# Kernel optimization log

Hardware: AMD Instinct MI355X
Metric: run time of the kernel (lower is better)

The kernel has to match this reference:

```python
import jax, jax.numpy as jnp
import numpy as np

B, T, FEATS, HEAD = 2, 2048, 2048, 16
DIM_HEAD = FEATS // HEAD
EPS = float(jnp.finfo(jnp.float32).eps)  # torch nn.RMSNorm default eps=None -> dtype eps


def _rms_norm(u, g):
    # u: [..., d]; torch RMSNorm: u / sqrt(mean(u^2) + eps) * g
    return u * jax.lax.rsqrt(jnp.mean(u * u, axis=-1, keepdims=True) + EPS) * g


def setup_inputs() -> dict:
    key = jax.random.key(0)
    kx, kw = jax.random.split(key)
    x = jax.random.normal(kx, (B, T, FEATS), dtype=jnp.float32)
    W = jax.random.normal(kw, (FEATS, FEATS), dtype=jnp.float32) / np.sqrt(FEATS)
    g1 = jnp.ones((DIM_HEAD,), dtype=jnp.float32)
    g2 = jnp.ones((DIM_HEAD,), dtype=jnp.float32)
    g3 = jnp.ones((DIM_HEAD,), dtype=jnp.float32)
    return {"x": x, "W": W, "g1": g1, "g2": g2, "g3": g3}


def reference(x, W, g1, g2, g3):
    Bb, Tt, C = x.shape
    sqrt_d = jnp.asarray(DIM_HEAD ** 0.5, dtype=x.dtype)
    # tied QKV projection: torch Linear -> x @ W.T ; then split heads -> [B,H,T,D]
    w = (x @ W.T).reshape(Bb, Tt, HEAD, DIM_HEAD).transpose(0, 2, 1, 3)
    q = _rms_norm(w, g1)
    k = _rms_norm(w, g2)
    v = _rms_norm(w, g3)
    att = jnp.einsum("bhid,bhjd->bhij", q, k) / sqrt_d  # [B,H,T,T]
    # symmetric row + column softmax
    score = jax.nn.softmax(att, axis=-1) + jax.nn.softmax(att, axis=-2)
    y = jnp.einsum("bhij,bhjd->bihd", score, v).reshape(Bb, Tt, C)
    # F.linear(y, W.t()) == y @ W  (tied-weight reprojection)
    return y @ W
```

## Files before the change

kernel.cpp:

```cpp
#include <hip/hip_runtime.h>
#include <stdint.h>

#define T_SEQ 2048
#define B_SZ 2
#define N_HEAD 16
#define D_HEAD 128
#define C_DIM 2048
#define M_ROWS (B_SZ*T_SEQ)
#define N_BH (B_SZ*N_HEAD)

typedef _Float16 f16;
typedef f16 f16x8 __attribute__((ext_vector_type(8)));
typedef f16 f16x4 __attribute__((ext_vector_type(4)));
typedef float f32x4 __attribute__((ext_vector_type(4)));

#define MFMA_F16(a,b,c) __builtin_amdgcn_mfma_f32_16x16x32_f16(a,b,c,0,0,0)

#define BAR_LGKM() do { asm volatile("s_waitcnt lgkmcnt(0)" ::: "memory"); \
                        __builtin_amdgcn_s_barrier(); } while (0)
#define BAR_ALL()  do { asm volatile("s_waitcnt vmcnt(0) lgkmcnt(0)" ::: "memory"); \
                        __builtin_amdgcn_s_barrier(); } while (0)

__device__ __forceinline__ float fexp2(float x) {
#if __has_builtin(__builtin_amdgcn_exp2f)
  return __builtin_amdgcn_exp2f(x);
#else
  float r; asm("v_exp_f32 %0, %1" : "=v"(r) : "v"(x)); return r;
#endif
}

__device__ __forceinline__ void gl_lds16(const void* g, void* l) {
  __builtin_amdgcn_global_load_lds(
      (const __attribute__((address_space(1))) unsigned int*)g,
      (__attribute__((address_space(3))) unsigned int*)l, 16, 0, 0);
}

#define MB_SCALE 0.12752924444069595f
#define RMS_EPS  1.1920928955078125e-07f

__global__ void k_prep(const float* __restrict__ W, const float* __restrict__ x,
                       f16* __restrict__ Wb, f16* __restrict__ Wtb,
                       f16* __restrict__ xb) {
  __shared__ float tile[64][65];
  const int lin = blockIdx.x;
  const int t = threadIdx.x;
  if (lin < 1024) {
    const int bx = (lin & 31) * 64;
    const int by = (lin >> 5) * 64;
    const int tc = t & 63, tr4 = t >> 6;
    for (int rr = tr4; rr < 64; rr += 4) {
      float v = W[(size_t)(by + rr) * C_DIM + bx + tc];
      tile[rr][tc] = v;
      Wb[(size_t)(by + rr) * C_DIM + bx + tc] = (f16)v;
    }
    __syncthreads();
    for (int rr = tr4; rr < 64; rr += 4) {
      Wtb[(size_t)(bx + rr) * C_DIM + by + tc] = (f16)tile[tc][rr];
    }
  } else {
    int i = (lin - 1024) * 256 + t;
    const int stride = 2048 * 256;
    const int n4 = (M_ROWS * C_DIM) / 4;
    for (; i < n4; i += stride) {
      f32x4 v = ((const f32x4*)x)[i];
      f16x4 o; o[0]=(f16)v[0]; o[1]=(f16)v[1]; o[2]=(f16)v[2]; o[3]=(f16)v[3];
      ((f16x4*)xb)[i] = o;
    }
  }
}

template<typename OT>
__global__ __launch_bounds__(256, 2)
void k_gemm_bt(const f16* __restrict__ A, const f16* __restrict__ Bm,
               OT* __restrict__ C, int Nd, int Kd) {
  __shared__ __align__(16) f16 As[2][128 * 64];
  __shared__ __align__(16) f16 Bs[2][128 * 64];
  const int tid = threadIdx.x;
  const int lane = tid & 63, wid = tid >> 6;
  const int lr = lane & 15, lkg = lane >> 4;
  const int wr = wid >> 1, wc = wid & 1;
  const int tm = blockIdx.y * 128, tn = blockIdx.x * 128;

  f32x4 acc[4][4];
#pragma unroll
  for (int i = 0; i < 4; ++i)
#pragma unroll
    for (int j = 0; j < 4; ++j) acc[i][j] = (f32x4){0.f, 0.f, 0.f, 0.f};

  const int nkt = Kd >> 6;

  auto stage = [&](int buf, int kt) {
    const int k0 = kt << 6;
    for (int s = 0; s < 4; ++s) {
      const int r0 = (wid * 4 + s) * 8;
      const int r = r0 + (lane >> 3);
      const int lg = ((lane & 7) ^ (r & 7)) << 3;
      gl_lds16(A + (size_t)(tm + r) * Kd + k0 + lg, &As[buf][r0 * 64]);
      gl_lds16(Bm + (size_t)(tn + r) * Kd + k0 + lg, &Bs[buf][r0 * 64]);
    }
  };

  stage(0, 0);
  int cur = 0;
  for (int kt = 0; kt < nkt; ++kt) {
    __syncthreads();
    if (kt + 1 < nkt) stage(cur ^ 1, kt + 1);
#pragma unroll
    for (int kk = 0; kk < 2; ++kk) {
      f16x8 a[4], b[4];
#pragma unroll
      for (int i = 0; i < 4; ++i) {
        const int ra = wr * 64 + i * 16 + lr;
        const int ga = ((kk * 4 + lkg) ^ (ra & 7)) << 3;
        a[i] = *(const f16x8*)&As[cur][ra * 64 + ga];
        const int rb = wc * 64 + i * 16 + lr;
        const int gb = ((kk * 4 + lkg) ^ (rb & 7)) << 3;
        b[i] = *(const f16x8*)&Bs[cur][rb * 64 + gb];
      }
#pragma unroll
      for (int i = 0; i < 4; ++i)
#pragma unroll
        for (int j = 0; j < 4; ++j) acc[i][j] = MFMA_F16(a[i], b[j], acc[i][j]);
    }
    cur ^= 1;
  }
#pragma unroll
  for (int i = 0; i < 4; ++i) {
    const int row0 = tm + wr * 64 + i * 16 + lkg * 4;
#pragma unroll
    for (int j = 0; j < 4; ++j) {
      const int col = tn + wc * 64 + j * 16 + lr;
#pragma unroll
      for (int r = 0; r < 4; ++r)
        C[(size_t)(row0 + r) * Nd + col] = (OT)acc[i][j][r];
    }
  }
}

__global__ __launch_bounds__(256, 2)
void k_gemm_qkv(const f16* __restrict__ A, const f16* __restrict__ Bm,
                const float* __restrict__ g1, const float* __restrict__ g2,
                f16* __restrict__ nb, f16* __restrict__ mb,
                f16* __restrict__ nT) {
  __shared__ __align__(16) char smem[70656];
  f16 (*As)[128 * 64] = (f16(*)[128 * 64])smem;
  f16 (*Bs)[128 * 64] = (f16(*)[128 * 64])(smem + 32768);
  f16* Cs = (f16*)smem;
  float* sc = (float*)(smem + 69632);

  const int tid = threadIdx.x;
  const int lane = tid & 63, wid = tid >> 6;
  const int lr = lane & 15, lkg = lane >> 4;
  const int wr = wid >> 1, wc = wid & 1;
  const int tm = blockIdx.y * 128;
  const int hh = blockIdx.x;
  const int tn = hh * 128;

  f32x4 acc[4][4];
#pragma unroll
  for (int i = 0; i < 4; ++i)
#pragma unroll
    for (int j = 0; j < 4; ++j) acc[i][j] = (f32x4){0.f, 0.f, 0.f, 0.f};

  auto stage = [&](int buf, int kt) {
    const int k0 = kt << 6;
    for (int s = 0; s < 4; ++s) {
      const int r0 = (wid * 4 + s) * 8;
      const int r = r0 + (lane >> 3);
      const int lg = ((lane & 7) ^ (r & 7)) << 3;
      gl_lds16(A + (size_t)(tm + r) * C_DIM + k0 + lg, &As[buf][r0 * 64]);
      gl_lds16(Bm + (size_t)(tn + r) * C_DIM + k0 + lg, &Bs[buf][r0 * 64]);
    }
  };

  stage(0, 0);
  int cur = 0;
  for (int kt = 0; kt < 32; ++kt) {
    __syncthreads();
    if (kt + 1 < 32) stage(cur ^ 1, kt + 1);
#pragma unroll
    for (int kk = 0; kk < 2; ++kk) {
      f16x8 a[4], b[4];
#pragma unroll
      for (int i = 0; i < 4; ++i) {
        const int ra = wr * 64 + i * 16 + lr;
        const int ga = ((kk * 4 + lkg) ^ (ra & 7)) << 3;
        a[i] = *(const f16x8*)&As[cur][ra * 64 + ga];
        const int rb = wc * 64 + i * 16 + lr;
        const int gb = ((kk * 4 + lkg) ^ (rb & 7)) << 3;
        b[i] = *(const f16x8*)&Bs[cur][rb * 64 + gb];
      }
#pragma unroll
      for (int i = 0; i < 4; ++i)
#pragma unroll
        for (int j = 0; j < 4; ++j) acc[i][j] = MFMA_F16(a[i], b[j], acc[i][j]);
    }
    cur ^= 1;
  }
  __syncthreads();

#pragma unroll
  for (int i = 0; i < 4; ++i)
#pragma unroll
    for (int j = 0; j < 4; ++j)
#pragma unroll
      for (int r = 0; r < 4; ++r)
        Cs[(wr * 64 + i * 16 + lkg * 4 + r) * 136 + wc * 64 + j * 16 + lr] =
            (f16)acc[i][j][r];
  __syncthreads();

  const int row = tid >> 1, dh = tid & 1;
  f16x8 v[8];
  float ss = 0.f;
#pragma unroll
  for (int c = 0; c < 8; ++c) {
    v[c] = *(const f16x8*)&Cs[row * 136 + dh * 64 + c * 8];
#pragma unroll
    for (int e = 0; e < 8; ++e) { float f = (float)v[c][e]; ss += f * f; }
  }
  ss += __shfl_xor(ss, 1);
  const float scale = rsqrtf(ss * (1.f / 128.f) + RMS_EPS);
  if (dh == 0) sc[row] = scale;

  const int grow = tm + row;
  const int b = grow >> 11, ts = grow & (T_SEQ - 1);
  const size_t nbase =
      ((size_t)((b * N_HEAD + hh) * T_SEQ + ts)) * 128 + dh * 64;
#pragma unroll
  for (int c = 0; c < 8; ++c) {
    const int d0 = dh * 64 + c * 8;
    f16x8 n8, m8;
#pragma unroll
    for (int e = 0; e < 8; ++e) {
      const float nf = (float)v[c][e] * scale;
      n8[e] = (f16)nf;
      m8[e] = (f16)(nf * g1[d0 + e] * g2[d0 + e] * MB_SCALE);
    }
    *(f16x8*)&nb[nbase + c * 8] = n8;
    *(f16x8*)&mb[nbase + c * 8] = m8;
  }
  __syncthreads();

  const int dcol = tid >> 1, th = tid & 1;
  const size_t tbase =
      ((size_t)((b * N_HEAD + hh) * 128 + dcol)) * T_SEQ + (tm & (T_SEQ - 1)) +
      th * 64;
#pragma unroll
  for (int rr = 0; rr < 8; ++rr) {
    f16x8 o;
#pragma unroll
    for (int e = 0; e < 8; ++e) {
      const int trow = th * 64 + rr * 8 + e;
      o[e] = (f16)((float)Cs[trow * 136 + dcol] * sc[trow]);
    }
    *(f16x8*)&nT[tbase + rr * 8] = o;
  }
}

__global__ __launch_bounds__(256, 2)
void k_stats_strip(const f16* __restrict__ mIn, const f16* __restrict__ nIn,
                   float* __restrict__ Ssum) {
  __shared__ __align__(16) f16 Ns[2][128 * 128];
  const int tid = threadIdx.x, lane = tid & 63, wid = tid >> 6;
  const int lr = lane & 15, lkg = lane >> 4;
  const int wr = wid >> 1, wc = wid & 1;
  const int p = blockIdx.x >> 1, h = blockIdx.x & 1;
  const int it1 = p, it2 = 15 - p;
  const int n1 = 16 - p;
  const int bh = blockIdx.y;
  const f16* mp = mIn + (size_t)bh * T_SEQ * 128;
  const f16* np = nIn + (size_t)bh * T_SEQ * 128;
  float* Sp = Ssum + (size_t)bh * T_SEQ;

  f16x8 msrW[2][4];
  auto loadMsr = [&](int itv) {
#pragma unroll
    for (int i = 0; i < 2; ++i)
#pragma unroll
      for (int kk = 0; kk < 4; ++kk)
        msrW[i][kk] = *(const f16x8*)&mp[(size_t)(itv * 128 + h * 64 + wr * 32 +
                                                  i * 16 + lr) * 128 +
                                         (kk * 4 + lkg) * 8];
  };
  auto stageN = [&](int buf, int jt) {
#pragma unroll
    for (int s = 0; s < 8; ++s) {
      const int r0 = (wid * 8 + s) * 4;
      const int r = r0 + (lane >> 4);
      const int lg = ((lane & 15) ^ (r & 7)) << 3;
      gl_lds16(np + (size_t)(jt * 128 + r) * 128 + lg, &Ns[buf][r0 * 128]);
    }
  };

  float rsum[8];
#pragma unroll
  for (int q = 0; q < 8; ++q) rsum[q] = 0.f;
  auto flushRows = [&](int itv) {
#pragma unroll
    for (int q = 0; q < 8; ++q) {
      float v = rsum[q];
      v += __shfl_xor(v, 1); v += __shfl_xor(v, 2);
      v += __shfl_xor(v, 4); v += __shfl_xor(v, 8);
      if (lr == 0) {
        const int row = itv * 128 + h * 64 + wr * 32 + (q >> 2) * 16 +
                        lkg * 4 + (q & 3);
        atomicAdd(&Sp[row], v);
      }
      rsum[q] = 0.f;
    }
  };

  loadMsr(it1);
  stageN(0, it1);
  BAR_ALL();
  int cur = 0;
  float csumP[4];
  int jtP = -1;

  for (int s = 0; s < 17; ++s) {
    const int itv = (s < n1) ? it1 : it2;
    const int jt = (s < n1) ? (it1 + s) : (it2 + (s - n1));
    if (s + 1 < 17) {
      const int jn = (s + 1 < n1) ? (it1 + s + 1) : (it2 + (s + 1 - n1));
      stageN(cur ^ 1, jn);
    }
    if (jtP >= 0) {
#pragma unroll
      for (int j = 0; j < 4; ++j)
        if (lkg == 0)
          atomicAdd(&Sp[jtP * 128 + wc * 64 + j * 16 + lr], csumP[j]);
      jtP = -1;
    }
    if (s == n1) { loadMsr(it2); flushRows(it1); }

    f32x4 acc[2][4];
#pragma unroll
    for (int i = 0; i < 2; ++i)
#pragma unroll
      for (int j = 0; j < 4; ++j) acc[i][j] = (f32x4){0.f, 0.f, 0.f, 0.f};
#pragma unroll
    for (int kk = 0; kk < 4; ++kk) {
      f16x8 b[4];
#pragma unroll
      for (int j = 0; j < 4; ++j) {
        const int rb = wc * 64 + j * 16 + lr;
        const int gb = ((kk * 4 + lkg) ^ (rb & 7)) << 3;
        b[j] = *(const f16x8*)&Ns[cur][rb * 128 + gb];
      }
#pragma unroll
      for (int i = 0; i < 2; ++i)
#pragma unroll
        for (int j = 0; j < 4; ++j)
          acc[i][j] = MFMA_F16(msrW[i][kk], b[j], acc[i][j]);
    }
    float cs[4];
#pragma unroll
    for (int j = 0; j < 4; ++j) cs[j] = 0.f;
#pragma unroll
    for (int i = 0; i < 2; ++i)
#pragma unroll
      for (int j = 0; j < 4; ++j)
#pragma unroll
        for (int r = 0; r < 4; ++r) {
          const float e = fexp2(acc[i][j][r]);
          rsum[i * 4 + r] += e;
          cs[j] += e;
        }
    if (jt != itv) {
#pragma unroll
      for (int j = 0; j < 4; ++j) {
        float v = cs[j];
        v += __shfl_xor(v, 16); v += __shfl_xor(v, 32);
        csumP[j] = v;
      }
      jtP = jt;
    }
    BAR_ALL();
    cur ^= 1;
  }
  if (jtP >= 0) {
#pragma unroll
    for (int j = 0; j < 4; ++j)
      if (lkg == 0)
        atomicAdd(&Sp[jtP * 128 + wc * 64 + j * 16 + lr], csumP[j]);
  }
  flushRows(it2);
}

__global__ void k_inv(const float* __restrict__ S, float* __restrict__ alpha) {
  const int i = blockIdx.x * blockDim.x + threadIdx.x;
  f32x4 s = ((const f32x4*)S)[i];
  f32x4 a;
#pragma unroll
  for (int e = 0; e < 4; ++e) a[e] = 1.f / s[e];
  ((f32x4*)alpha)[i] = a;
}

__global__ __launch_bounds__(256, 2)
void k_apply(const f16* __restrict__ mIn, const f16* __restrict__ nIn,
             const f16* __restrict__ nTIn, const float* __restrict__ alpha,
             const float* __restrict__ g3, f16* __restrict__ yb) {
  __shared__ __align__(16) f16 Ns[2][64 * 128];
  __shared__ __align__(16) f16 Nts[2][128 * 64];
  __shared__ __align__(16) f16 Ps[128 * 64];
  const int tid = threadIdx.x, lane = tid & 63, wid = tid >> 6;
  const int lr = lane & 15, lkg = lane >> 4;
  const int wj = wid >> 1;
  const int wi = wid & 1;
  const int lin = blockIdx.x + (blockIdx.y << 4);
  const int swz = ((lin & 7) << 6) + (lin >> 3);
  const int it = swz & 15, bh = swz >> 4;
  const int b = bh >> 4, hh = bh & 15;
  const f16* mp = mIn + (size_t)bh * T_SEQ * 128;
  const f16* np = nIn + (size_t)bh * T_SEQ * 128;
  const f16* ntp = nTIn + (size_t)bh * 128 * T_SEQ;
  const float* al = alpha + (size_t)bh * T_SEQ;

  f16x8 msr[4][4];
#pragma unroll
  for (int ii = 0; ii < 4; ++ii)
#pragma unroll
    for (int kk = 0; kk < 4; ++kk)
      msr[ii][kk] = *(const f16x8*)&mp[(size_t)(it * 128 + wi * 64 + ii * 16 + lr) * 128 +
                                       (kk * 4 + lkg) * 8];

  auto stageN = [&](int buf, int jt) {
#pragma unroll
    for (int s = 0; s < 4; ++s) {
      const int r0 = (wid * 4 + s) * 4;
      const int r = r0 + (lane >> 4);
      const int lg = ((lane & 15) ^ (r & 7)) << 3;
      gl_lds16(np + (size_t)(jt * 64 + r) * 128 + lg, &Ns[buf][r0 * 128]);
    }
  };
  auto stageNT = [&](int buf, int jt) {
#pragma unroll
    for (int s = 0; s < 4; ++s) {
      const int r0 = (wid * 4 + s) * 8;
      const int r = r0 + (lane >> 3);
      const int lg = ((lane & 7) ^ (r & 7)) << 3;
      gl_lds16(ntp + (size_t)r * T_SEQ + jt * 64 + lg, &Nts[buf][r0 * 64]);
    }
  };

  float ai[4];
#pragma unroll
  for (int ii = 0; ii < 4; ++ii) ai[ii] = al[it * 128 + wi * 64 + ii * 16 + lr];

  f32x4 yacc[4][4];
#pragma unroll
  for (int i = 0; i < 4; ++i)
#pragma unroll
    for (int j = 0; j < 4; ++j) yacc[i][j] = (f32x4){0.f, 0.f, 0.f, 0.f};

  stageN(0, 0);
  stageNT(0, 0);
  BAR_ALL();
  int cur = 0;
  for (int jt = 0; jt < 32; ++jt) {
    float aj[8];
#pragma unroll
    for (int jj = 0; jj < 2; ++jj)
#pragma unroll
      for (int r = 0; r < 4; ++r)
        aj[jj * 4 + r] = al[jt * 64 + wj * 32 + jj * 16 + lkg * 4 + r];
    if (jt < 31) { stageN(cur ^ 1, jt + 1); stageNT(cur ^ 1, jt + 1); }

    f32x4 acc[2][4];
#pragma unroll
    for (int i = 0; i < 2; ++i)
#pragma unroll
      for (int j = 0; j < 4; ++j) acc[i][j] = (f32x4){0.f, 0.f, 0.f, 0.f};
#pragma unroll
    for (int kk = 0; kk < 4; ++kk) {
      f16x8 a[2];
#pragma unroll
      for (int jj = 0; jj < 2; ++jj) {
        const int jrow = wj * 32 + jj * 16 + lr;
        a[jj] = *(const f16x8*)&Ns[cur][jrow * 128 + (((kk * 4 + lkg) ^ (jrow & 7)) << 3)];
      }
#pragma unroll
      for (int jj = 0; jj < 2; ++jj)
#pragma unroll
        for (int ii = 0; ii < 4; ++ii)
          acc[jj][ii] = MFMA_F16(a[jj], msr[ii][kk], acc[jj][ii]);
    }

#pragma unroll
    for (int jj = 0; jj < 2; ++jj)
#pragma unroll
      for (int ii = 0; ii < 4; ++ii) {
        f16x4 o;
#pragma unroll
        for (int r = 0; r < 4; ++r) {
          const float p = fexp2(acc[jj][ii][r]) * (ai[ii] + aj[jj * 4 + r]);
          o[r] = (f16)p;
        }
        const int il = wi * 64 + ii * 16 + lr;
        const int jl = wj * 32 + jj * 16 + lkg * 4;
        *(f16x4*)&Ps[il * 64 + (((jl >> 3) ^ (il & 7)) << 3) + (jl & 7)] = o;
      }
    BAR_LGKM();

#pragma unroll
    for (int kk = 0; kk < 2; ++kk) {
      f16x8 a[4], bfr[4];
#pragma unroll
      for (int dd = 0; dd < 4; ++dd) {
        const int drow = wj * 64 + dd * 16 + lr;
        a[dd] = *(const f16x8*)&Nts[cur][drow * 64 + (((kk * 4 + lkg) ^ (drow & 7)) << 3)];
      }
#pragma unroll
      for (int ii = 0; ii < 4; ++ii) {
        const int irow = wi * 64 + ii * 16 + lr;
        bfr[ii] = *(const f16x8*)&Ps[irow * 64 + (((kk * 4 + lkg) ^ (irow & 7)) << 3)];
      }
#pragma unroll
      for (int dd = 0; dd < 4; ++dd)
#pragma unroll
        for (int ii = 0; ii < 4; ++ii)
          yacc[dd][ii] = MFMA_F16(a[dd], bfr[ii], yacc[dd][ii]);
    }
    BAR_ALL();
    cur ^= 1;
  }

#pragma unroll
  for (int dd = 0; dd < 4; ++dd) {
    const int d0 = wj * 64 + dd * 16 + lkg * 4;
    float g3v[4];
#pragma unroll
    for (int r = 0; r < 4; ++r) g3v[r] = g3[d0 + r];
#pragma unroll
    for (int ii = 0; ii < 4; ++ii) {
      const int icol = wi * 64 + ii * 16 + lr;
      const size_t base =
          ((size_t)(b * T_SEQ + it * 128 + icol)) * C_DIM + hh * 128 + d0;
      f16x4 o;
#pragma unroll
      for (int r = 0; r < 4; ++r) o[r] = (f16)(yacc[dd][ii][r] * g3v[r]);
      *(f16x4*)&yb[base] = o;
    }
  }
}

extern "C" void kernel_launch(void* const* d_in, const int* in_sizes, int n_in,
                              void* d_out, int out_size, void* d_ws,
                              size_t ws_size, hipStream_t stream) {
  const float* x = (const float*)d_in[0];
  const float* W = (const float*)d_in[1];
  const float* g1 = (const float*)d_in[2];
  const float* g2 = (const float*)d_in[3];
  const float* g3 = (const float*)d_in[4];
  float* out = (float*)d_out;
  char* ws = (char*)d_ws;

  f16* xb   = (f16*)(ws);
  f16* Wb   = (f16*)(ws + 16777216);
  f16* Wtb  = (f16*)(ws + 25165824);
  f16* nb   = (f16*)(ws + 50331648);
  f16* mb   = (f16*)(ws + 67108864);
  f16* nT   = (f16*)(ws + 83886080);
  f16* yb   = (f16*)(ws + 100663296);
  float* alpha = (float*)(ws + 117440512);
  float* Ssum  = (float*)(ws + 117702656);

  hipMemsetAsync(Ssum, 0, 262144, stream);
  k_prep<<<dim3(3072), 256, 0, stream>>>(W, x, Wb, Wtb, xb);
  k_gemm_qkv<<<dim3(16, 32), 256, 0, stream>>>(xb, Wb, g1, g2, nb, mb, nT);
  k_stats_strip<<<dim3(16, 32), 256, 0, stream>>>(mb, nb, Ssum);
  k_inv<<<dim3(64), 256, 0, stream>>>(Ssum, alpha);
  k_apply<<<dim3(16, 32), 256, 0, stream>>>(mb, nb, nT, alpha, g3, yb);
  k_gemm_bt<float><<<dim3(16, 32), 256, 0, stream>>>(yb, Wtb, out, C_DIM, C_DIM);
}
```

Measured before the change: 240.8 us.

## Split stats strip work by tile steps instead of row halves

The stats kernel previously had each of two blocks per pair cover half of the 128 query rows across all 17 key tiles, so both blocks staged every key tile. Now each block covers all 128 rows of the query tile but only half of the 17 steps (9 and 8). This halves the key-tile staging per block and doubles the MFMA work per staged tile. In exchange each thread holds twice the query fragments and accumulators, which raises register pressure and may reduce occupancy. The split is also uneven, 9 steps against 8.

```diff
diff --git a/kernel.cpp b/kernel.cpp
--- a/kernel.cpp
+++ b/kernel.cpp
@@ -258,8 +258,8 @@
 }
 
 __global__ __launch_bounds__(256, 2)
-void k_stats_strip(const f16* __restrict__ mIn, const f16* __restrict__ nIn,
-                   float* __restrict__ Ssum) {
+void k_stats_tri2(const f16* __restrict__ mIn, const f16* __restrict__ nIn,
+                  float* __restrict__ Ssum) {
   __shared__ __align__(16) f16 Ns[2][128 * 128];
   const int tid = threadIdx.x, lane = tid & 63, wid = tid >> 6;
   const int lr = lane & 15, lkg = lane >> 4;
@@ -267,20 +267,20 @@
   const int p = blockIdx.x >> 1, h = blockIdx.x & 1;
   const int it1 = p, it2 = 15 - p;
   const int n1 = 16 - p;
+  const int s0 = h ? 9 : 0, s1 = h ? 17 : 9;
   const int bh = blockIdx.y;
   const f16* mp = mIn + (size_t)bh * T_SEQ * 128;
   const f16* np = nIn + (size_t)bh * T_SEQ * 128;
   float* Sp = Ssum + (size_t)bh * T_SEQ;
 
-  f16x8 msrW[2][4];
+  f16x8 msrW[4][4];
   auto loadMsr = [&](int itv) {
 #pragma unroll
-    for (int i = 0; i < 2; ++i)
+    for (int i = 0; i < 4; ++i)
 #pragma unroll
       for (int kk = 0; kk < 4; ++kk)
-        msrW[i][kk] = *(const f16x8*)&mp[(size_t)(itv * 128 + h * 64 + wr * 32 +
-                                                  i * 16 + lr) * 128 +
-                                         (kk * 4 + lkg) * 8];
+        msrW[i][kk] = *(const f16x8*)&mp[(size_t)(itv * 128 + wr * 64 + i * 16 +
+                                                  lr) * 128 + (kk * 4 + lkg) * 8];
   };
   auto stageN = [&](int buf, int jt) {
 #pragma unroll
@@ -292,38 +292,37 @@
     }
   };
 
-  float rsum[8];
-#pragma unroll
-  for (int q = 0; q < 8; ++q) rsum[q] = 0.f;
+  float rsum[16];
+#pragma unroll
+  for (int q = 0; q < 16; ++q) rsum[q] = 0.f;
   auto flushRows = [&](int itv) {
 #pragma unroll
-    for (int q = 0; q < 8; ++q) {
+    for (int q = 0; q < 16; ++q) {
       float v = rsum[q];
       v += __shfl_xor(v, 1); v += __shfl_xor(v, 2);
       v += __shfl_xor(v, 4); v += __shfl_xor(v, 8);
       if (lr == 0) {
-        const int row = itv * 128 + h * 64 + wr * 32 + (q >> 2) * 16 +
-                        lkg * 4 + (q & 3);
+        const int row = itv * 128 + wr * 64 + (q >> 2) * 16 + lkg * 4 + (q & 3);
         atomicAdd(&Sp[row], v);
       }
       rsum[q] = 0.f;
     }
   };
-
-  loadMsr(it1);
-  stageN(0, it1);
+  auto tileOf = [&](int s) { return (s < n1) ? (it1 + s) : (it2 + (s - n1)); };
+  auto itOf = [&](int s) { return (s < n1) ? it1 : it2; };
+
+  int cur_it = itOf(s0);
+  loadMsr(cur_it);
+  stageN(0, tileOf(s0));
   BAR_ALL();
   int cur = 0;
   float csumP[4];
   int jtP = -1;
 
-  for (int s = 0; s < 17; ++s) {
-    const int itv = (s < n1) ? it1 : it2;
-    const int jt = (s < n1) ? (it1 + s) : (it2 + (s - n1));
-    if (s + 1 < 17) {
-      const int jn = (s + 1 < n1) ? (it1 + s + 1) : (it2 + (s + 1 - n1));
-      stageN(cur ^ 1, jn);
-    }
+  for (int s = s0; s < s1; ++s) {
+    const int itv = itOf(s);
+    const int jt = tileOf(s);
+    if (s + 1 < s1) stageN(cur ^ 1, tileOf(s + 1));
     if (jtP >= 0) {
 #pragma unroll
       for (int j = 0; j < 4; ++j)
@@ -331,11 +330,11 @@
           atomicAdd(&Sp[jtP * 128 + wc * 64 + j * 16 + lr], csumP[j]);
       jtP = -1;
     }
-    if (s == n1) { loadMsr(it2); flushRows(it1); }
-
-    f32x4 acc[2][4];
-#pragma unroll
-    for (int i = 0; i < 2; ++i)
+    if (itv != cur_it) { loadMsr(itv); flushRows(cur_it); cur_it = itv; }
+
+    f32x4 acc[4][4];
+#pragma unroll
+    for (int i = 0; i < 4; ++i)
 #pragma unroll
       for (int j = 0; j < 4; ++j) acc[i][j] = (f32x4){0.f, 0.f, 0.f, 0.f};
 #pragma unroll
@@ -348,7 +347,7 @@
         b[j] = *(const f16x8*)&Ns[cur][rb * 128 + gb];
       }
 #pragma unroll
-      for (int i = 0; i < 2; ++i)
+      for (int i = 0; i < 4; ++i)
 #pragma unroll
         for (int j = 0; j < 4; ++j)
           acc[i][j] = MFMA_F16(msrW[i][kk], b[j], acc[i][j]);
@@ -357,7 +356,7 @@
 #pragma unroll
     for (int j = 0; j < 4; ++j) cs[j] = 0.f;
 #pragma unroll
-    for (int i = 0; i < 2; ++i)
+    for (int i = 0; i < 4; ++i)
 #pragma unroll
       for (int j = 0; j < 4; ++j)
 #pragma unroll
@@ -384,7 +383,7 @@
       if (lkg == 0)
         atomicAdd(&Sp[jtP * 128 + wc * 64 + j * 16 + lr], csumP[j]);
   }
-  flushRows(it2);
+  flushRows(cur_it);
 }
 
 __global__ void k_inv(const float* __restrict__ S, float* __restrict__ alpha) {
@@ -568,7 +567,7 @@
   hipMemsetAsync(Ssum, 0, 262144, stream);
   k_prep<<<dim3(3072), 256, 0, stream>>>(W, x, Wb, Wtb, xb);
   k_gemm_qkv<<<dim3(16, 32), 256, 0, stream>>>(xb, Wb, g1, g2, nb, mb, nT);
-  k_stats_strip<<<dim3(16, 32), 256, 0, stream>>>(mb, nb, Ssum);
+  k_stats_tri2<<<dim3(16, 32), 256, 0, stream>>>(mb, nb, Ssum);
   k_inv<<<dim3(64), 256, 0, stream>>>(Ssum, alpha);
   k_apply<<<dim3(16, 32), 256, 0, stream>>>(mb, nb, nT, alpha, g3, yb);
   k_gemm_bt<float><<<dim3(16, 32), 256, 0, stream>>>(yb, Wtb, out, C_DIM, C_DIM);
```

Result: faster. 233.5 us (-3.0%).
